# Kernel optimization log

Hardware: AMD Instinct MI355X
Metric: run time of the kernel (lower is better)

The kernel has to match this reference:

```python
import jax, jax.numpy as jnp
import numpy as np

DIM = 1024
HEADS = 16
HEAD_DIM = DIM // HEADS
B, N = 2, 2048


def setup_inputs() -> dict:
    key = jax.random.key(0)
    k1, k2, k3, k4 = jax.random.split(key, 4)
    scale = 1.0 / np.sqrt(DIM)
    return {
        "x": jax.random.normal(k1, (B, N, DIM), dtype=jnp.float32),
        "w_qkv": jax.random.normal(k2, (DIM, 3 * DIM), dtype=jnp.float32) * scale,
        "w_out": jax.random.normal(k3, (DIM, DIM), dtype=jnp.float32) * scale,
        "b_out": jax.random.normal(k4, (DIM,), dtype=jnp.float32) * 0.01,
    }


def reference(x, w_qkv, w_out, b_out):
    b, n, c = x.shape
    h, d = HEADS, c // HEADS
    sm_scale = d ** -0.5
    qkv = x @ w_qkv  # [b, n, 3c]
    q, k, v = jnp.split(qkv, 3, axis=-1)
    # [b, n, c] -> [b, h, n, d]
    q = q.reshape(b, n, h, d).transpose(0, 2, 1, 3)
    k = k.reshape(b, n, h, d).transpose(0, 2, 1, 3)
    v = v.reshape(b, n, h, d).transpose(0, 2, 1, 3)
    dots = jnp.einsum("bhqd,bhkd->bhqk", q, k) * sm_scale
    attn = jax.nn.softmax(dots, axis=-1)
    out = jnp.einsum("bhqk,bhkd->bhqd", attn, v)
    out = out.transpose(0, 2, 1, 3).reshape(b, n, c)
    return out @ w_out + b_out
```

## Files before the change

kernel.cpp:

```cpp
#include <hip/hip_runtime.h>
#include <hip/hip_bf16.h>

typedef __attribute__((ext_vector_type(8))) short bf16x8;
typedef __attribute__((ext_vector_type(4))) float f32x4;

#define B_    2
#define N_    2048
#define DIM_  1024
#define H_    16
#define D_    64
#define BH_   32
#define QSC   0.18033688f

static __device__ __forceinline__ void gload_lds16(const void* g, void* l) {
  __builtin_amdgcn_global_load_lds((const __attribute__((address_space(1))) void*)g,
                                   (__attribute__((address_space(3))) void*)l, 16, 0, 0);
}

__global__ __launch_bounds__(256) void prep_kernel(const float* __restrict__ x,
                                                   const float* __restrict__ w_qkv,
                                                   const float* __restrict__ w_out,
                                                   __hip_bfloat16* __restrict__ xb,
                                                   __hip_bfloat16* __restrict__ wqkT,
                                                   __hip_bfloat16* __restrict__ woT) {
  __shared__ float tile[64][65];
  const int bid = blockIdx.x, t = threadIdx.x;
  if (bid < 4096) {
    const int i = bid * 256 + t;
    float4 v = reinterpret_cast<const float4*>(x)[i];
    union { __hip_bfloat16 h[4]; uint2 u; } cv;
    cv.h[0] = __float2bfloat16(v.x);
    cv.h[1] = __float2bfloat16(v.y);
    cv.h[2] = __float2bfloat16(v.z);
    cv.h[3] = __float2bfloat16(v.w);
    reinterpret_cast<uint2*>(xb)[i] = cv.u;
    return;
  }
  const float* in;
  __hip_bfloat16* out;
  int R, C, c0, r0;
  if (bid < 4096 + 768) {
    const int bx = bid - 4096;
    in = w_qkv; out = wqkT; R = 1024; C = 3072;
    c0 = (bx % 48) * 64; r0 = (bx / 48) * 64;
  } else {
    const int bx = bid - 4096 - 768;
    in = w_out; out = woT; R = 1024; C = 1024;
    c0 = (bx % 16) * 64; r0 = (bx / 16) * 64;
  }
#pragma unroll
  for (int i = 0; i < 16; ++i) {
    int idx = i * 256 + t;
    int r = idx >> 6, c = idx & 63;
    tile[r][c] = in[(size_t)(r0 + r) * C + (c0 + c)];
  }
  __syncthreads();
#pragma unroll
  for (int i = 0; i < 16; ++i) {
    int idx = i * 256 + t;
    int rr = idx >> 6, cc = idx & 63;
    out[(size_t)(c0 + rr) * R + (r0 + cc)] = __float2bfloat16(tile[cc][rr]);
  }
}

#define GEMM_CORE(A_, Bt_)                                                               \
  constexpr int K = 1024;                                                                \
  __shared__ __align__(16) __hip_bfloat16 As[128 * 64];                                  \
  __shared__ __align__(16) __hip_bfloat16 Bs[128 * 64];                                  \
  const int t = threadIdx.x, w = t >> 6, lane = t & 63;                                  \
  const int l16 = lane & 15, kg = lane >> 4;                                             \
  const int m0 = blockIdx.y * 128, n0 = blockIdx.x * 128;                                \
  const int wm = w >> 1, wn = w & 1;                                                     \
  f32x4 acc[4][4];                                                                       \
  _Pragma("unroll") for (int i = 0; i < 4; ++i)                                          \
    _Pragma("unroll") for (int j = 0; j < 4; ++j) acc[i][j] = {0.f, 0.f, 0.f, 0.f};      \
                \
  size_t srcA[4], srcB[4];                                                               \
  _Pragma("unroll") for (int i = 0; i < 4; ++i) {                                        \
    const int c = 256 * i + t;                                                           \
    const int row = c >> 3, jsw = (c & 7) ^ (row & 7);                                   \
    srcA[i] = (size_t)(m0 + row) * K + jsw * 8;                                          \
    srcB[i] = (size_t)(n0 + row) * K + jsw * 8;                                          \
  }                                                                                      \
  for (int k0 = 0; k0 < K; k0 += 64) {                                                   \
    __syncthreads();                                                                     \
    _Pragma("unroll") for (int i = 0; i < 4; ++i) {                                      \
      gload_lds16(A_ + srcA[i] + k0, (char*)As + 4096 * i + 1024 * w);                   \
      gload_lds16(Bt_ + srcB[i] + k0, (char*)Bs + 4096 * i + 1024 * w);                  \
    }                                                                                    \
    __syncthreads();                                                                     \
    _Pragma("unroll") for (int kk = 0; kk < 2; ++kk) {                                   \
      bf16x8 a[4], b[4];                                                                 \
      _Pragma("unroll") for (int i = 0; i < 4; ++i) {                                    \
        const int row = wm * 64 + i * 16 + l16;                                          \
        const int jsw = ((kk << 2) | kg) ^ (row & 7);                                    \
        a[i] = *reinterpret_cast<const bf16x8*>((const char*)As + row * 128 + jsw * 16); \
      }                                                                                  \
      _Pragma("unroll") for (int j = 0; j < 4; ++j) {                                    \
        const int row = wn * 64 + j * 16 + l16;                                          \
        const int jsw = ((kk << 2) | kg) ^ (row & 7);                                    \
        b[j] = *reinterpret_cast<const bf16x8*>((const char*)Bs + row * 128 + jsw * 16); \
      }                                                                                  \
      _Pragma("unroll") for (int i = 0; i < 4; ++i)                                      \
        _Pragma("unroll") for (int j = 0; j < 4; ++j)                                    \
          acc[i][j] = __builtin_amdgcn_mfma_f32_16x16x32_bf16(a[i], b[j], acc[i][j], 0, 0, 0); \
    }                                                                                    \
  }

__global__ __launch_bounds__(256) void gemm_qkv_kernel(const __hip_bfloat16* __restrict__ A,
                                                       const __hip_bfloat16* __restrict__ Bt,
                                                       __hip_bfloat16* __restrict__ Qw,
                                                       __hip_bfloat16* __restrict__ Kw,
                                                       __hip_bfloat16* __restrict__ Vt) {
  GEMM_CORE(A, Bt)

#pragma unroll
  for (int j = 0; j < 4; ++j) {
    const int n = n0 + wn * 64 + j * 16 + l16;
    const int which = n >> 10, nn = n & 1023;
    const int h = nn >> 6, d = nn & 63;
#pragma unroll
    for (int i = 0; i < 4; ++i) {
      const int m = m0 + wm * 64 + i * 16 + kg * 4;
      const int bb = m >> 11, tt = m & 2047;
      if (which == 2) {
        union { __hip_bfloat16 hh[4]; unsigned long long u; } pv;
#pragma unroll
        for (int r = 0; r < 4; ++r) pv.hh[r] = __float2bfloat16(acc[i][j][r]);
        *reinterpret_cast<unsigned long long*>(
            &Vt[((size_t)(bb * H_ + h) * D_ + d) * N_ + tt]) = pv.u;
      } else {
        __hip_bfloat16* dst = (which == 0) ? Qw : Kw;
        const float sc = (which == 0) ? QSC : 1.0f;
#pragma unroll
        for (int r = 0; r < 4; ++r)
          dst[((size_t)(bb * H_ + h) * N_ + tt + r) * D_ + d] = __float2bfloat16(acc[i][j][r] * sc);
      }
    }
  }
}

__global__ __launch_bounds__(256) void gemm_out_kernel(const __hip_bfloat16* __restrict__ A,
                                                       const __hip_bfloat16* __restrict__ Bt,
                                                       const float* __restrict__ bo,
                                                       float* __restrict__ out) {
  GEMM_CORE(A, Bt)

#pragma unroll
  for (int j = 0; j < 4; ++j) {
    const int n = n0 + wn * 64 + j * 16 + l16;
    const float bias = bo[n];
#pragma unroll
    for (int i = 0; i < 4; ++i) {
#pragma unroll
      for (int r = 0; r < 4; ++r) {
        const int m = m0 + wm * 64 + i * 16 + kg * 4 + r;
        out[(size_t)m * 1024 + n] = acc[i][j][r] + bias;
      }
    }
  }
}

__global__ __launch_bounds__(512) void attn_kernel(const __hip_bfloat16* __restrict__ Q,
                                                   const __hip_bfloat16* __restrict__ K,
                                                   const __hip_bfloat16* __restrict__ Vt,
                                                   __hip_bfloat16* __restrict__ O) {
  __shared__ __align__(16) __hip_bfloat16 Ks[2][64 * 64];
  __shared__ __align__(16) __hip_bfloat16 Vs[2][64 * 64];
  __shared__ __align__(16) __hip_bfloat16 Plds[8][16][64];
  const int bh = blockIdx.y;
  const int q0 = blockIdx.x * 128;
  const int t = threadIdx.x, w = t >> 6, lane = t & 63;
  const int l16 = lane & 15, kg = lane >> 4;
  const int b = bh >> 4, h = bh & 15;

  const __hip_bfloat16* Kbh = K + (size_t)bh * N_ * D_;
  const __hip_bfloat16* Vbh = Vt + (size_t)bh * D_ * N_;

  const int crow = t >> 3, cb = t & 7;
  const int csw = cb ^ (crow & 7);
  const size_t offK = (size_t)crow * D_ + csw * 8;
  const size_t offV = (size_t)crow * N_ + csw * 8;

  const __hip_bfloat16* Qp = Q + ((size_t)bh * N_ + q0 + w * 16 + l16) * D_ + kg * 8;
  const bf16x8 qf0 = *reinterpret_cast<const bf16x8*>(Qp);
  const bf16x8 qf1 = *reinterpret_cast<const bf16x8*>(Qp + 32);

  bf16x8 ones;
#pragma unroll
  for (int i = 0; i < 8; ++i) ones[i] = (short)0x3F80;

  f32x4 oaccS = {0.f, 0.f, 0.f, 0.f};
  f32x4 oacc[4];
#pragma unroll
  for (int dn = 0; dn < 4; ++dn) oacc[dn] = {0.f, 0.f, 0.f, 0.f};

#define STAGE(bufi, kv)                                                          \
  do {                                                                           \
    gload_lds16(Kbh + (size_t)(kv) * D_ + offK, (char*)Ks[bufi] + w * 1024);     \
    gload_lds16(Vbh + (kv) + offV,              (char*)Vs[bufi] + w * 1024);     \
  } while (0)

  STAGE(0, 0);
  asm volatile("s_waitcnt vmcnt(0)" ::: "memory");
  __builtin_amdgcn_s_barrier();

#pragma unroll 1
  for (int it = 0; it < N_ / 64; ++it) {
    const int buf = it & 1;
    if (it + 1 < N_ / 64) STAGE(buf ^ 1, (it + 1) * 64);

    const char* Kb = (const char*)Ks[buf];
    const char* Vb = (const char*)Vs[buf];

    f32x4 s[4];
#pragma unroll
    for (int kt = 0; kt < 4; ++kt) s[kt] = {0.f, 0.f, 0.f, 0.f};
    __builtin_amdgcn_s_setprio(1);
#pragma unroll
    for (int kt = 0; kt < 4; ++kt) {
      const int row = kt * 16 + l16;
      const int rsw = (row & 7) << 4;
      const bf16x8 k0 = *reinterpret_cast<const bf16x8*>(Kb + row * 128 + ((kg << 4) ^ rsw));
      const bf16x8 k1 = *reinterpret_cast<const bf16x8*>(Kb + row * 128 + (((4 + kg) << 4) ^ rsw));
      s[kt] = __builtin_amdgcn_mfma_f32_16x16x32_bf16(k0, qf0, s[kt], 0, 0, 0);
      s[kt] = __builtin_amdgcn_mfma_f32_16x16x32_bf16(k1, qf1, s[kt], 0, 0, 0);
    }
    __builtin_amdgcn_s_setprio(0);

    const int xm3 = (l16 & 7) << 3;
#pragma unroll
    for (int kt = 0; kt < 4; ++kt) {
      union { __hip_bfloat16 hh[4]; unsigned long long u; } pk;
#pragma unroll
      for (int r = 0; r < 4; ++r) pk.hh[r] = __float2bfloat16(__builtin_amdgcn_exp2f(s[kt][r]));
      *reinterpret_cast<unsigned long long*>(&Plds[w][l16][(16 * kt + 4 * kg) ^ xm3]) = pk.u;
    }

    __builtin_amdgcn_s_setprio(1);
#pragma unroll
    for (int kk = 0; kk < 2; ++kk) {
      const bf16x8 pa = *reinterpret_cast<const bf16x8*>(
          &Plds[w][l16][(kk * 32 + kg * 8) ^ xm3]);
      oaccS = __builtin_amdgcn_mfma_f32_16x16x32_bf16(pa, ones, oaccS, 0, 0, 0);
#pragma unroll
      for (int dn = 0; dn < 4; ++dn) {
        const int vrow = dn * 16 + l16;
        const int vsw = (vrow & 7) << 4;
        const bf16x8 vf = *reinterpret_cast<const bf16x8*>(
            Vb + vrow * 128 + ((kk * 64 + kg * 16) ^ vsw));
        oacc[dn] = __builtin_amdgcn_mfma_f32_16x16x32_bf16(pa, vf, oacc[dn], 0, 0, 0);
      }
    }
    __builtin_amdgcn_s_setprio(0);

    asm volatile("s_waitcnt vmcnt(0)" ::: "memory");
    __builtin_amdgcn_s_barrier();
  }
#undef STAGE

  float inv[4];
#pragma unroll
  for (int r = 0; r < 4; ++r) inv[r] = 1.0f / oaccS[r];
  __hip_bfloat16* Ob = O + ((size_t)b * N_ + q0 + w * 16) * DIM_ + h * D_;
#pragma unroll
  for (int dn = 0; dn < 4; ++dn)
#pragma unroll
    for (int r = 0; r < 4; ++r)
      Ob[(size_t)(kg * 4 + r) * DIM_ + dn * 16 + l16] = __float2bfloat16(oacc[dn][r] * inv[r]);
}

extern "C" void kernel_launch(void* const* d_in, const int* in_sizes, int n_in,
                              void* d_out, int out_size, void* d_ws, size_t ws_size,
                              hipStream_t stream) {
  const float* x = (const float*)d_in[0];
  const float* w_qkv = (const float*)d_in[1];
  const float* w_out = (const float*)d_in[2];
  const float* b_out = (const float*)d_in[3];
  float* out = (float*)d_out;

  __hip_bfloat16* ws = (__hip_bfloat16*)d_ws;
  __hip_bfloat16* xb = ws;
  __hip_bfloat16* wqkT = xb + (size_t)4096 * 1024;
  __hip_bfloat16* woT = wqkT + (size_t)3072 * 1024;
  __hip_bfloat16* Qw = woT + (size_t)1024 * 1024;
  __hip_bfloat16* Kw = Qw + (size_t)BH_ * N_ * D_;
  __hip_bfloat16* Vt = Kw + (size_t)BH_ * N_ * D_;
  __hip_bfloat16* Ow = Vt + (size_t)BH_ * N_ * D_;

  prep_kernel<<<5120, 256, 0, stream>>>(x, w_qkv, w_out, xb, wqkT, woT);
  gemm_qkv_kernel<<<dim3(24, 32), 256, 0, stream>>>(xb, wqkT, Qw, Kw, Vt);
  attn_kernel<<<dim3(16, 32), 512, 0, stream>>>(Qw, Kw, Vt, Ow);
  gemm_out_kernel<<<dim3(8, 32), 256, 0, stream>>>(Ow, woT, b_out, out);
}
```

Before: 122.6 us.

## Rewrite QKV GEMM with 256x256 tiles, double-buffered async LDS pipeline

The QKV projection GEMM moves from 128x128 tiles with 256 threads and synchronous single-buffer loads to 256x256 tiles with 512 threads, 128KB of double-buffered LDS, and global-to-LDS prefetch of the next K tile spread across four MFMA phases. It also remaps block indices so neighbouring blocks share input tiles in cache, and raises wave priority during MFMA bursts. The aim is to hide load latency behind compute and raise operand reuse per LDS byte. In exchange, the grid shrinks to 192 blocks on a chip with more CUs, register pressure rises, and LDS use limits occupancy.

```diff
diff --git a/kernel.cpp b/kernel.cpp
--- a/kernel.cpp
+++ b/kernel.cpp
@@ -74,7 +74,6 @@
   f32x4 acc[4][4];                                                                       \
   _Pragma("unroll") for (int i = 0; i < 4; ++i)                                          \
     _Pragma("unroll") for (int j = 0; j < 4; ++j) acc[i][j] = {0.f, 0.f, 0.f, 0.f};      \
-                \
   size_t srcA[4], srcB[4];                                                               \
   _Pragma("unroll") for (int i = 0; i < 4; ++i) {                                        \
     const int c = 256 * i + t;                                                           \
@@ -107,26 +106,122 @@
     }                                                                                    \
   }
 
-__global__ __launch_bounds__(256) void gemm_qkv_kernel(const __hip_bfloat16* __restrict__ A,
-                                                       const __hip_bfloat16* __restrict__ Bt,
-                                                       __hip_bfloat16* __restrict__ Qw,
-                                                       __hip_bfloat16* __restrict__ Kw,
-                                                       __hip_bfloat16* __restrict__ Vt) {
-  GEMM_CORE(A, Bt)
-
-#pragma unroll
-  for (int j = 0; j < 4; ++j) {
-    const int n = n0 + wn * 64 + j * 16 + l16;
-    const int which = n >> 10, nn = n & 1023;
+__global__ __launch_bounds__(512, 2) void gemm_qkv_kernel(const __hip_bfloat16* __restrict__ A,
+                                                          const __hip_bfloat16* __restrict__ Bt,
+                                                          __hip_bfloat16* __restrict__ Qw,
+                                                          __hip_bfloat16* __restrict__ Kw,
+                                                          __hip_bfloat16* __restrict__ Vt) {
+  __shared__ __align__(16) char lds[131072];
+  const int t = threadIdx.x, w = t >> 6, lane = t & 63;
+  const int l16 = lane & 15, kg = lane >> 4;
+  int flat = blockIdx.y * 12 + blockIdx.x;
+  flat = (flat & 7) * 24 + (flat >> 3);
+  const int bx = flat % 12, by = flat / 12;
+  const int m0 = by * 256, n0 = bx * 256;
+  const int wm = w >> 2, wn = w & 3;
+  const int rA = t >> 3;
+  const int jb = (t & 7) ^ (rA & 7);
+
+#define LDSOFF(bb, mat) (((bb) * 2 + (mat)) * 32768)
+#define STG_A(bb, tt, h)                                                                    \
+  do {                                                                                      \
+    gload_lds16(A + (size_t)(m0 + rA + 64 * (h)) * 1024 + (tt) * 64 + jb * 8,               \
+                (char*)lds + LDSOFF(bb, 0) + (h) * 8192 + t * 16);                          \
+    gload_lds16(A + (size_t)(m0 + rA + 64 * (h) + 128) * 1024 + (tt) * 64 + jb * 8,         \
+                (char*)lds + LDSOFF(bb, 0) + (h) * 8192 + 16384 + t * 16);                  \
+  } while (0)
+#define STG_B(bb, tt, h)                                                                    \
+  do {                                                                                      \
+    gload_lds16(Bt + (size_t)(n0 + rA + 128 * (h)) * 1024 + (tt) * 64 + jb * 8,             \
+                (char*)lds + LDSOFF(bb, 1) + (h) * 16384 + t * 16);                         \
+    gload_lds16(Bt + (size_t)(n0 + rA + 128 * (h) + 64) * 1024 + (tt) * 64 + jb * 8,        \
+                (char*)lds + LDSOFF(bb, 1) + (h) * 16384 + 8192 + t * 16);                  \
+  } while (0)
+#define RD_A(dst, q, i, kk)                                                                 \
+  {                                                                                         \
+    const int row = wm * 128 + ((q) * 2 + (i)) * 16 + l16;                                  \
+    dst = *reinterpret_cast<const bf16x8*>(Ab + row * 128 + ((((kk) * 4 + kg) ^ (row & 7)) * 16)); \
+  }
+#define RD_B(dst, nj, kk)                                                                   \
+  {                                                                                         \
+    const int row = wn * 64 + (nj) * 16 + l16;                                              \
+    dst = *reinterpret_cast<const bf16x8*>(Bb + row * 128 + ((((kk) * 4 + kg) ^ (row & 7)) * 16)); \
+  }
+#define PHASE(q)                                                                            \
+  do {                                                                                      \
+    bf16x8 af[2][2];                                                                        \
+    _Pragma("unroll") for (int i = 0; i < 2; ++i)                                           \
+      _Pragma("unroll") for (int kk = 0; kk < 2; ++kk) RD_A(af[i][kk], q, i, kk);           \
+    __builtin_amdgcn_s_setprio(1);                                                          \
+    _Pragma("unroll") for (int i = 0; i < 2; ++i)                                           \
+      _Pragma("unroll") for (int nj = 0; nj < 4; ++nj)                                      \
+        _Pragma("unroll") for (int kk = 0; kk < 2; ++kk)                                    \
+          acc[(q) * 2 + i][nj] =                                                            \
+              __builtin_amdgcn_mfma_f32_16x16x32_bf16(af[i][kk], bfr[nj][kk],               \
+                                                      acc[(q) * 2 + i][nj], 0, 0, 0);       \
+    __builtin_amdgcn_s_setprio(0);                                                          \
+  } while (0)
+
+  f32x4 acc[8][4];
+#pragma unroll
+  for (int i = 0; i < 8; ++i)
+#pragma unroll
+    for (int j = 0; j < 4; ++j) acc[i][j] = {0.f, 0.f, 0.f, 0.f};
+
+  STG_A(0, 0, 0); STG_A(0, 0, 1); STG_B(0, 0, 0); STG_B(0, 0, 1);
+  STG_B(1, 1, 0); STG_B(1, 1, 1); STG_A(1, 1, 0);
+
+#pragma unroll 1
+  for (int kt = 0; kt < 16; ++kt) {
+    const int b = kt & 1;
+    const char* Ab = (const char*)lds + LDSOFF(b, 0);
+    const char* Bb = (const char*)lds + LDSOFF(b, 1);
+
+    if (kt < 15) STG_A(b ^ 1, kt + 1, 1);
+    __builtin_amdgcn_sched_barrier(0);
+    if (kt < 15) asm volatile("s_waitcnt vmcnt(8)" ::: "memory");
+    else         asm volatile("s_waitcnt vmcnt(0)" ::: "memory");
+    __builtin_amdgcn_s_barrier();
+    __builtin_amdgcn_sched_barrier(0);
+    bf16x8 bfr[4][2];
+#pragma unroll
+    for (int nj = 0; nj < 4; ++nj)
+#pragma unroll
+      for (int kk = 0; kk < 2; ++kk) RD_B(bfr[nj][kk], nj, kk);
+    PHASE(0);
+    __builtin_amdgcn_s_barrier();
+    __builtin_amdgcn_sched_barrier(0);
+
+    if (kt < 14) STG_B(b, kt + 2, 0);
+    __builtin_amdgcn_sched_barrier(0);
+    PHASE(1);
+    __builtin_amdgcn_s_barrier();
+    __builtin_amdgcn_sched_barrier(0);
+
+    if (kt < 14) STG_B(b, kt + 2, 1);
+    PHASE(2);
+
+    if (kt < 14) STG_A(b, kt + 2, 0);
+    __builtin_amdgcn_sched_barrier(0);
+    PHASE(3);
+    __builtin_amdgcn_s_barrier();
+    __builtin_amdgcn_sched_barrier(0);
+  }
+
+  const int which = n0 >> 10;
+#pragma unroll
+  for (int nj = 0; nj < 4; ++nj) {
+    const int n = n0 + wn * 64 + nj * 16 + l16;
+    const int nn = n & 1023;
     const int h = nn >> 6, d = nn & 63;
 #pragma unroll
-    for (int i = 0; i < 4; ++i) {
-      const int m = m0 + wm * 64 + i * 16 + kg * 4;
+    for (int mi = 0; mi < 8; ++mi) {
+      const int m = m0 + wm * 128 + mi * 16 + kg * 4;
       const int bb = m >> 11, tt = m & 2047;
       if (which == 2) {
         union { __hip_bfloat16 hh[4]; unsigned long long u; } pv;
 #pragma unroll
-        for (int r = 0; r < 4; ++r) pv.hh[r] = __float2bfloat16(acc[i][j][r]);
+        for (int r = 0; r < 4; ++r) pv.hh[r] = __float2bfloat16(acc[mi][nj][r]);
         *reinterpret_cast<unsigned long long*>(
             &Vt[((size_t)(bb * H_ + h) * D_ + d) * N_ + tt]) = pv.u;
       } else {
@@ -134,10 +229,16 @@
         const float sc = (which == 0) ? QSC : 1.0f;
 #pragma unroll
         for (int r = 0; r < 4; ++r)
-          dst[((size_t)(bb * H_ + h) * N_ + tt + r) * D_ + d] = __float2bfloat16(acc[i][j][r] * sc);
+          dst[((size_t)(bb * H_ + h) * N_ + tt + r) * D_ + d] = __float2bfloat16(acc[mi][nj][r] * sc);
       }
     }
   }
+#undef PHASE
+#undef RD_B
+#undef RD_A
+#undef STG_B
+#undef STG_A
+#undef LDSOFF
 }
 
 __global__ __launch_bounds__(256) void gemm_out_kernel(const __hip_bfloat16* __restrict__ A,
@@ -289,7 +390,7 @@
   __hip_bfloat16* Ow = Vt + (size_t)BH_ * N_ * D_;
 
   prep_kernel<<<5120, 256, 0, stream>>>(x, w_qkv, w_out, xb, wqkT, woT);
-  gemm_qkv_kernel<<<dim3(24, 32), 256, 0, stream>>>(xb, wqkT, Qw, Kw, Vt);
+  gemm_qkv_kernel<<<dim3(12, 16), 512, 0, stream>>>(xb, wqkT, Qw, Kw, Vt);
   attn_kernel<<<dim3(16, 32), 512, 0, stream>>>(Qw, Kw, Vt, Ow);
   gemm_out_kernel<<<dim3(8, 32), 256, 0, stream>>>(Ow, woT, b_out, out);
 }
```

Result: faster. 115.3 us (-5.9%).
